# Kernel optimization log

Hardware: AMD Instinct MI355X
Metric: run time of the kernel (lower is better)

The kernel has to match this reference:

```python
import jax, jax.numpy as jnp
import numpy as np

B, T, E, H, V = 4, 2048, 1024, 16, 32000
HD = E // H  # head_dim = 64


def setup_inputs() -> dict:
    key = jax.random.key(0)
    ks = jax.random.split(key, 16)
    s = 0.02
    p = lambda k, shp: jax.random.normal(k, shp, jnp.float32) * s
    return {
        "x": jax.random.randint(ks[0], (B, T), 0, V),
        "tok_emb": p(ks[1], (V, E)),
        "pos_emb": p(ks[2], (T, E)),
        "m_Wq": p(ks[3], (E, E)), "m_Wk": p(ks[4], (E, E)),
        "m_Wv": p(ks[5], (E, E)), "m_Wo": p(ks[6], (E, E)),
        "m_bo": jnp.zeros((E,), jnp.float32),
        "h_Wq": p(ks[7], (E, E)), "h_Wk": p(ks[8], (E, E)),
        "h_Wv": p(ks[9], (E, E)), "h_Wo": p(ks[10], (E, E)),
        "h_bo": jnp.zeros((E,), jnp.float32),
        "f_W1": p(ks[11], (E, 512)), "f_b1": jnp.zeros((512,), jnp.float32),
        "f_W2": p(ks[12], (512, 1024)), "f_b2": jnp.zeros((1024,), jnp.float32),
        "f_W3": p(ks[13], (1024, 512)), "f_b3": jnp.zeros((512,), jnp.float32),
        "f_W4": p(ks[14], (512, E)), "f_b4": jnp.zeros((E,), jnp.float32),
        "ln_g": jnp.ones((E,), jnp.float32),
        "ln_b": jnp.zeros((E,), jnp.float32),
    }


def _layernorm(x, g, b, eps=1e-5):
    m = x.mean(-1, keepdims=True)
    v = ((x - m) ** 2).mean(-1, keepdims=True)
    return (x - m) / jnp.sqrt(v + eps) * g + b


def _mha(x, Wq, Wk, Wv, Wo, bo, masked):
    b, t, e = x.shape
    # [b, t, e] -> [b, h, t, hd]
    q = (x @ Wq).reshape(b, t, H, HD).transpose(0, 2, 1, 3)
    k = (x @ Wk).reshape(b, t, H, HD).transpose(0, 2, 1, 3)
    v = (x @ Wv).reshape(b, t, H, HD).transpose(0, 2, 1, 3)
    wei = jnp.einsum("bhqd,bhkd->bhqk", q, k) / np.float32(np.sqrt(HD))
    if masked:  # causal (module is in training mode by default)
        causal = jnp.tril(jnp.ones((t, t), dtype=bool))
        wei = jnp.where(causal, wei, -jnp.inf)
    att = jax.nn.softmax(wei, axis=-1)
    out = jnp.einsum("bhqk,bhkd->bhqd", att, v).transpose(0, 2, 1, 3).reshape(b, t, e)
    return out @ Wo + bo


def _ffn(x, W1, b1, W2, b2, W3, b3, W4, b4):
    h = jax.nn.relu(x @ W1 + b1)
    h = jax.nn.relu(h @ W2 + b2)
    h = jax.nn.relu(h @ W3 + b3)
    return h @ W4 + b4


def reference(x, tok_emb, pos_emb,
              m_Wq, m_Wk, m_Wv, m_Wo, m_bo,
              h_Wq, h_Wk, h_Wv, h_Wo, h_bo,
              f_W1, f_b1, f_W2, f_b2, f_W3, f_b3, f_W4, f_b4,
              ln_g, ln_b):
    e = tok_emb[x] + pos_emb[jnp.arange(x.shape[1])]          # [B, T, E]
    r = _layernorm(e + _mha(e, m_Wq, m_Wk, m_Wv, m_Wo, m_bo, True), ln_g, ln_b)
    r = _layernorm(r + _mha(r, h_Wq, h_Wk, h_Wv, h_Wo, h_bo, False), ln_g, ln_b)
    r = _layernorm(r + _ffn(r, f_W1, f_b1, f_W2, f_b2, f_W3, f_b3, f_W4, f_b4), ln_g, ln_b)
    return r
```

## Files before the change

### kernel.cpp

```cpp
#include <hip/hip_runtime.h>
#include <hip/hip_bf16.h>


typedef __attribute__((ext_vector_type(8))) short v8s;
typedef __attribute__((ext_vector_type(4))) short v4s;
typedef __attribute__((ext_vector_type(4))) float v4f;
typedef __attribute__((ext_vector_type(16))) float v16f;
typedef __attribute__((ext_vector_type(4))) unsigned int v4u;

#define MFMA16(a, b, c) __builtin_amdgcn_mfma_f32_16x16x32_bf16((a), (b), (c), 0, 0, 0)
#define MFMA32(a, b, c) __builtin_amdgcn_mfma_f32_32x32x16_bf16((a), (b), (c), 0, 0, 0)

typedef const __attribute__((address_space(1))) void* gas1_t;
typedef __attribute__((address_space(3))) void* las3_t;

__device__ __forceinline__ void gl_lds16(const void* g, void* l) {
  __builtin_amdgcn_global_load_lds((gas1_t)g, (las3_t)l, 16, 0, 0);
}

__device__ __forceinline__ unsigned short f2bf(float f) {
  __hip_bfloat16 h = __float2bfloat16(f);
  return *reinterpret_cast<unsigned short*>(&h);
}

__device__ __forceinline__ float bf2f(unsigned short u) {
  union { unsigned int i; float f; } v;
  v.i = (unsigned int)u << 16;
  return v.f;
}

__device__ __forceinline__ float fast_exp2(float x) {
  float r;
  asm("v_exp_f32 %0, %1" : "=v"(r) : "v"(x));
  return r;
}

__device__ __forceinline__ unsigned int cvt_pk_bf16(float lo, float hi) {
  unsigned int r;
  asm("v_cvt_pk_bf16_f32 %0, %1, %2" : "=v"(r) : "v"(lo), "v"(hi));
  return r;
}

__device__ __forceinline__ float max3f(float a, float b, float c) {
  float r;
  asm("v_max3_f32 %0, %1, %2, %3" : "=v"(r) : "v"(a), "v"(b), "v"(c));
  return r;
}

#define QSCALE 0.18033688011112042f

struct TransDesc {
  const float* src[12];
  unsigned short* dst[12];
};

__global__ __launch_bounds__(256)
void transpose_all(TransDesc td) {
  const int bid = blockIdx.x;
  int m, tile, K, N;
  if (bid < 8192) { m = bid >> 10; tile = bid & 1023; K = 1024; N = 1024; }
  else {
    const int r = bid - 8192;
    m = 8 + (r >> 9); tile = r & 511;
    if (m & 1) { K = 512; N = 1024; } else { K = 1024; N = 512; }
  }
  const float* src = td.src[m];
  unsigned short* dst = td.dst[m];
  const int ntx = N >> 5;
  const int n0 = (tile % ntx) * 32, k0 = (tile / ntx) * 32;

  __shared__ float tile_s[32][33];
  const int tx = threadIdx.x & 31, ty = threadIdx.x >> 5;
#pragma unroll
  for (int i = 0; i < 32; i += 8)
    tile_s[ty + i][tx] = src[(size_t)(k0 + ty + i) * N + n0 + tx];
  __syncthreads();
#pragma unroll
  for (int i = 0; i < 32; i += 8)
    dst[(size_t)(n0 + ty + i) * K + k0 + tx] = f2bf(tile_s[tx][ty + i]);
}

__global__ __launch_bounds__(256)
void embed_k(const int* __restrict__ x, const float* __restrict__ tok,
             const float* __restrict__ pos, unsigned short* __restrict__ act) {
  const int t = blockIdx.x, tid = threadIdx.x;
  const int id = x[t], tp = t & 2047;
  float4 v = ((const float4*)(tok + (size_t)id * 1024))[tid];
  float4 p = ((const float4*)(pos + (size_t)tp * 1024))[tid];
  ushort4 u;
  u.x = f2bf(v.x + p.x); u.y = f2bf(v.y + p.y);
  u.z = f2bf(v.z + p.z); u.w = f2bf(v.w + p.w);
  ((ushort4*)(act + (size_t)t * 1024))[tid] = u;
}

__global__ __launch_bounds__(256)
void gemm_bt(const unsigned short* __restrict__ A, const unsigned short* __restrict__ Bt,
             const float* __restrict__ bias, void* __restrict__ C,
             int M, int N, int K, int flags) {
  __shared__ __align__(16) unsigned short As[128 * 64];
  __shared__ __align__(16) unsigned short Bs[128 * 64];
  const int tid = threadIdx.x;
  const int w = tid >> 6, l = tid & 63;
  const int l31 = l & 31, l5 = l >> 5;
  const int wm = w & 1, wn = w >> 1;
  const int m0 = blockIdx.x * 128, n0 = blockIdx.y * 128;
  const int ra = l >> 3, ka = ((l & 7) ^ (l >> 3)) * 8;
  const int fswz = (l31 & 7) * 8;

  v16f acc[2][2];
#pragma unroll
  for (int bm = 0; bm < 2; ++bm)
#pragma unroll
    for (int bn = 0; bn < 2; ++bn)
#pragma unroll
      for (int r = 0; r < 16; ++r) acc[bm][bn][r] = 0.f;

  for (int k0 = 0; k0 < K; k0 += 64) {
#pragma unroll
    for (int i = 0; i < 4; ++i) {
      const int c = w + i * 4;
      gl_lds16(A  + (size_t)(m0 + c * 8 + ra) * K + k0 + ka, &As[c * 512]);
      gl_lds16(Bt + (size_t)(n0 + c * 8 + ra) * K + k0 + ka, &Bs[c * 512]);
    }
    __syncthreads();
#pragma unroll
    for (int kk = 0; kk < 4; ++kk) {
      const int co = (kk * 16 + l5 * 8) ^ fswz;
      const v8s a0 = *(const v8s*)&As[(wm * 64 + l31) * 64 + co];
      const v8s a1 = *(const v8s*)&As[(wm * 64 + 32 + l31) * 64 + co];
      const v8s b0 = *(const v8s*)&Bs[(wn * 64 + l31) * 64 + co];
      const v8s b1 = *(const v8s*)&Bs[(wn * 64 + 32 + l31) * 64 + co];
      acc[0][0] = MFMA32(a0, b0, acc[0][0]);
      acc[0][1] = MFMA32(a0, b1, acc[0][1]);
      acc[1][0] = MFMA32(a1, b0, acc[1][0]);
      acc[1][1] = MFMA32(a1, b1, acc[1][1]);
    }
    __syncthreads();
  }

  const bool relu = flags & 1, obf = flags & 2, qs = flags & 4;
#pragma unroll
  for (int bn = 0; bn < 2; ++bn) {
    const int col = n0 + wn * 64 + bn * 32 + l31;
    const float bv = bias ? bias[col] : 0.f;
    const float sc = (qs && col < 1024) ? QSCALE : 1.f;
#pragma unroll
    for (int bm = 0; bm < 2; ++bm) {
      const int rowbase = m0 + wm * 64 + bm * 32 + 4 * l5;
#pragma unroll
      for (int r = 0; r < 16; ++r) {
        const int row = rowbase + (r & 3) + 8 * (r >> 2);
        float v = (acc[bm][bn][r] + bv) * sc;
        if (relu) v = fmaxf(v, 0.f);
        if (obf) ((unsigned short*)C)[(size_t)row * N + col] = f2bf(v);
        else     ((float*)C)[(size_t)row * N + col] = v;
      }
    }
  }
}

#define LDQ 3072
template <bool CAUSAL>
__global__ __launch_bounds__(512)
void flash_attn(const unsigned short* __restrict__ qkv, unsigned short* __restrict__ O) {
  __shared__ __align__(16) unsigned short Kt[64 * 64];
  __shared__ __align__(16) unsigned short Vt[64 * 64];
  const int tid = threadIdx.x;
  const int w = tid >> 6, l = tid & 63, lr = l & 15, lg = l >> 4;
  const int b = blockIdx.y >> 4, h = blockIdx.y & 15;
  const size_t baseq = ((size_t)b * 2048) * LDQ + h * 64;
  const size_t baseo = ((size_t)b * 2048) * 1024 + h * 64;
  const int kswz = (lr & 7) * 8;
  const int vswz = lr * 4;

  const int kra = l >> 3, kka = ((l & 7) ^ (l >> 3)) * 8;
  const int vp_ = tid & 31, vd0 = ((tid >> 5) & 7) * 8;

  const int nq = CAUSAL ? 2 : 1;
  for (int qi = 0; qi < nq; ++qi) {
    const int qt = CAUSAL ? (qi ? 15 - (int)blockIdx.x : (int)blockIdx.x)
                          : (int)blockIdx.x;
    const int q0w = qt * 128 + w * 16;

    const unsigned short* qp = qkv + baseq + (size_t)(q0w + lr) * LDQ + lg * 8;
    const v8s qf0 = *(const v8s*)qp;
    const v8s qf1 = *(const v8s*)(qp + 32);

    v4f acc[4];
    const v4f vzero = {0.f, 0.f, 0.f, 0.f};
#pragma unroll
    for (int n = 0; n < 4; ++n) acc[n] = vzero;
    float mrow = -INFINITY, lrow = 0.f;

    const int kv_end = CAUSAL ? qt * 128 + 128 : 2048;
    for (int kv0 = 0; kv0 < kv_end; kv0 += 64) {
      if (w >= 4) {
#pragma unroll
        for (int i = 0; i < 2; ++i) {
          const int c = (w - 4) * 2 + i;
          gl_lds16(qkv + baseq + 1024 + (size_t)(kv0 + c * 8 + kra) * LDQ + kka,
                   &Kt[c * 512]);
        }
      } else {
        const unsigned short* va = qkv + baseq + 2048 + (size_t)(kv0 + 2 * vp_) * LDQ + vd0;
        const v8s v0 = *(const v8s*)va;
        const v8s v1 = *(const v8s*)(va + LDQ);
#pragma unroll
        for (int j = 0; j < 8; ++j) {
          const unsigned int pk = (unsigned int)(unsigned short)v0[j] |
                                  ((unsigned int)(unsigned short)v1[j] << 16);
          *(unsigned int*)&Vt[(vd0 + j) * 64 + ((2 * vp_) ^ (((vd0 + j) & 15) * 4))] = pk;
        }
      }
      __syncthreads();

      v4f s[4];
#pragma unroll
      for (int n = 0; n < 4; ++n) s[n] = vzero;
      __builtin_amdgcn_s_setprio(1);
#pragma unroll
      for (int kk = 0; kk < 2; ++kk) {
#pragma unroll
        for (int n = 0; n < 4; ++n) {
          const v8s kf = *(const v8s*)&Kt[(n * 16 + lr) * 64 + ((kk * 32 + lg * 8) ^ kswz)];
          s[n] = MFMA16(kf, kk ? qf1 : qf0, s[n]);
        }
      }
      __builtin_amdgcn_s_setprio(0);

      if (CAUSAL && (kv0 + 63 > q0w)) {
        const int qg = q0w + lr;
#pragma unroll
        for (int n = 0; n < 4; ++n) {
          const int kvb = kv0 + n * 16 + lg * 4;
#pragma unroll
          for (int r = 0; r < 4; ++r)
            if (kvb + r > qg) s[n][r] = -INFINITY;
        }
      }

      float tm;
      {
        const float t0 = max3f(s[0][0], s[0][1], s[0][2]);
        const float t1 = max3f(s[0][3], s[1][0], s[1][1]);
        const float t2 = max3f(s[1][2], s[1][3], s[2][0]);
        const float t3 = max3f(s[2][1], s[2][2], s[2][3]);
        const float t4 = max3f(s[3][0], s[3][1], s[3][2]);
        tm = max3f(t0, t1, s[3][3]);
        tm = max3f(tm, t2, t3);
        tm = fmaxf(tm, t4);
      }
      tm = fmaxf(tm, __shfl_xor(tm, 16));
      tm = fmaxf(tm, __shfl_xor(tm, 32));

      if (__any(tm > mrow + 8.f)) {
        const float mn = fmaxf(mrow, tm);
        const float fac = fast_exp2(mrow - mn);
        mrow = mn;
        lrow *= fac;
        float facT[4];
#pragma unroll
        for (int r = 0; r < 4; ++r)
          facT[r] = __shfl(fac, (l & 48) | (lg * 4 + r));
#pragma unroll
        for (int n = 0; n < 4; ++n)
#pragma unroll
          for (int r = 0; r < 4; ++r) acc[n][r] *= facT[r];
      }

      float rs = 0.f;
#pragma unroll
      for (int n = 0; n < 4; ++n)
#pragma unroll
        for (int r = 0; r < 4; ++r) {
          s[n][r] = fast_exp2(s[n][r] - mrow);
          rs += s[n][r];
        }
      rs += __shfl_xor(rs, 16);
      rs += __shfl_xor(rs, 32);
      lrow += rs;

      v4u pu0, pu1;
      pu0.x = cvt_pk_bf16(s[0][0], s[0][1]); pu0.y = cvt_pk_bf16(s[0][2], s[0][3]);
      pu0.z = cvt_pk_bf16(s[1][0], s[1][1]); pu0.w = cvt_pk_bf16(s[1][2], s[1][3]);
      pu1.x = cvt_pk_bf16(s[2][0], s[2][1]); pu1.y = cvt_pk_bf16(s[2][2], s[2][3]);
      pu1.z = cvt_pk_bf16(s[3][0], s[3][1]); pu1.w = cvt_pk_bf16(s[3][2], s[3][3]);
      v8s pf0, pf1;
      __builtin_memcpy(&pf0, &pu0, 16);
      __builtin_memcpy(&pf1, &pu1, 16);

      __builtin_amdgcn_s_setprio(1);
#pragma unroll
      for (int kk = 0; kk < 2; ++kk) {
#pragma unroll
        for (int n = 0; n < 4; ++n) {
          const int rowb = (n * 16 + lr) * 64;
          const v4s va_ = *(const v4s*)&Vt[rowb + ((kk * 32 + lg * 4) ^ vswz)];
          const v4s vb_ = *(const v4s*)&Vt[rowb + ((kk * 32 + 16 + lg * 4) ^ vswz)];
          const v8s vf = __builtin_shufflevector(va_, vb_, 0, 1, 2, 3, 4, 5, 6, 7);
          acc[n] = MFMA16(kk ? pf1 : pf0, vf, acc[n]);
        }
      }
      __builtin_amdgcn_s_setprio(0);
      __syncthreads();
    }

    float lT[4];
#pragma unroll
    for (int r = 0; r < 4; ++r)
      lT[r] = __shfl(lrow, (l & 48) | (lg * 4 + r));
#pragma unroll
    for (int n = 0; n < 4; ++n)
#pragma unroll
      for (int r = 0; r < 4; ++r) {
        const float v = acc[n][r] / lT[r];
        O[baseo + (size_t)(q0w + lg * 4 + r) * 1024 + n * 16 + lr] = f2bf(v);
      }
  }
}

__global__ __launch_bounds__(256)
void add_ln(const unsigned short* __restrict__ ra, const unsigned short* __restrict__ rb,
            const float* __restrict__ g, const float* __restrict__ be,
            unsigned short* __restrict__ ob, float* __restrict__ of) {
  const int t = blockIdx.x, tid = threadIdx.x;
  const ushort4 ua = ((const ushort4*)(ra + (size_t)t * 1024))[tid];
  const ushort4 ub = ((const ushort4*)(rb + (size_t)t * 1024))[tid];
  float4 s;
  s.x = bf2f(ua.x) + bf2f(ub.x);
  s.y = bf2f(ua.y) + bf2f(ub.y);
  s.z = bf2f(ua.z) + bf2f(ub.z);
  s.w = bf2f(ua.w) + bf2f(ub.w);
  float sum = s.x + s.y + s.z + s.w;
  float sq  = s.x * s.x + s.y * s.y + s.z * s.z + s.w * s.w;
#pragma unroll
  for (int off = 32; off > 0; off >>= 1) {
    sum += __shfl_xor(sum, off);
    sq  += __shfl_xor(sq, off);
  }
  __shared__ float red[8];
  const int w = tid >> 6;
  if ((tid & 63) == 0) { red[w] = sum; red[4 + w] = sq; }
  __syncthreads();
  sum = red[0] + red[1] + red[2] + red[3];
  sq  = red[4] + red[5] + red[6] + red[7];
  const float mean = sum * (1.f / 1024.f);
  const float var  = sq * (1.f / 1024.f) - mean * mean;
  const float rstd = rsqrtf(var + 1e-5f);
  const float4 gg = ((const float4*)g)[tid];
  const float4 bb = ((const float4*)be)[tid];
  float4 y;
  y.x = (s.x - mean) * rstd * gg.x + bb.x;
  y.y = (s.y - mean) * rstd * gg.y + bb.y;
  y.z = (s.z - mean) * rstd * gg.z + bb.z;
  y.w = (s.w - mean) * rstd * gg.w + bb.w;
  if (ob) {
    ushort4 u;
    u.x = f2bf(y.x); u.y = f2bf(y.y); u.z = f2bf(y.z); u.w = f2bf(y.w);
    ((ushort4*)(ob + (size_t)t * 1024))[tid] = u;
  }
  if (of) ((float4*)(of + (size_t)t * 1024))[tid] = y;
}

extern "C" void kernel_launch(void* const* d_in, const int* in_sizes, int n_in,
                              void* d_out, int out_size, void* d_ws, size_t ws_size,
                              hipStream_t stream) {
  const int*   x    = (const int*)d_in[0];
  const float* tok  = (const float*)d_in[1];
  const float* pos  = (const float*)d_in[2];
  const float* mWq  = (const float*)d_in[3];
  const float* mWk  = (const float*)d_in[4];
  const float* mWv  = (const float*)d_in[5];
  const float* mWo  = (const float*)d_in[6];
  const float* m_bo = (const float*)d_in[7];
  const float* hWq  = (const float*)d_in[8];
  const float* hWk  = (const float*)d_in[9];
  const float* hWv  = (const float*)d_in[10];
  const float* hWo  = (const float*)d_in[11];
  const float* h_bo = (const float*)d_in[12];
  const float* fW1  = (const float*)d_in[13];
  const float* f_b1 = (const float*)d_in[14];
  const float* fW2  = (const float*)d_in[15];
  const float* f_b2 = (const float*)d_in[16];
  const float* fW3  = (const float*)d_in[17];
  const float* f_b3 = (const float*)d_in[18];
  const float* fW4  = (const float*)d_in[19];
  const float* f_b4 = (const float*)d_in[20];
  const float* ln_g = (const float*)d_in[21];
  const float* ln_b = (const float*)d_in[22];

  char* ws = (char*)d_ws;
  const size_t MB = 1ull << 20;
  unsigned short* wqkv1 = (unsigned short*)(ws + 0 * MB);
  unsigned short* wqkv2 = (unsigned short*)(ws + 6 * MB);
  unsigned short* wo1   = (unsigned short*)(ws + 12 * MB);
  unsigned short* wo2   = (unsigned short*)(ws + 14 * MB);
  unsigned short* fW1_t = (unsigned short*)(ws + 16 * MB);
  unsigned short* fW2_t = (unsigned short*)(ws + 17 * MB);
  unsigned short* fW3_t = (unsigned short*)(ws + 18 * MB);
  unsigned short* fW4_t = (unsigned short*)(ws + 19 * MB);
  unsigned short* actA  = (unsigned short*)(ws + 20 * MB);
  unsigned short* actB  = (unsigned short*)(ws + 36 * MB);
  unsigned short* tmp   = (unsigned short*)(ws + 52 * MB);
  unsigned short* qkv   = (unsigned short*)(ws + 68 * MB);
  unsigned short* h1    = (unsigned short*)(ws + 68 * MB);
  unsigned short* h2    = (unsigned short*)(ws + 76 * MB);
  unsigned short* h3    = (unsigned short*)(ws + 92 * MB);
  unsigned short* attno = (unsigned short*)(ws + 116 * MB);

  TransDesc td;
  td.src[0] = mWq; td.dst[0] = wqkv1;
  td.src[1] = mWk; td.dst[1] = wqkv1 + 1024 * 1024;
  td.src[2] = mWv; td.dst[2] = wqkv1 + 2048 * 1024;
  td.src[3] = mWo; td.dst[3] = wo1;
  td.src[4] = hWq; td.dst[4] = wqkv2;
  td.src[5] = hWk; td.dst[5] = wqkv2 + 1024 * 1024;
  td.src[6] = hWv; td.dst[6] = wqkv2 + 2048 * 1024;
  td.src[7] = hWo; td.dst[7] = wo2;
  td.src[8] = fW1; td.dst[8] = fW1_t;
  td.src[9] = fW2; td.dst[9] = fW2_t;
  td.src[10] = fW3; td.dst[10] = fW3_t;
  td.src[11] = fW4; td.dst[11] = fW4_t;
  transpose_all<<<10240, 256, 0, stream>>>(td);

  embed_k<<<8192, 256, 0, stream>>>(x, tok, pos, actA);

  gemm_bt<<<dim3(64, 24), 256, 0, stream>>>(actA, wqkv1, nullptr, qkv, 8192, 3072, 1024, 6);
  flash_attn<true><<<dim3(8, 64), 512, 0, stream>>>(qkv, attno);
  gemm_bt<<<dim3(64, 8), 256, 0, stream>>>(attno, wo1, m_bo, tmp, 8192, 1024, 1024, 2);
  add_ln<<<8192, 256, 0, stream>>>(actA, tmp, ln_g, ln_b, actB, nullptr);

  gemm_bt<<<dim3(64, 24), 256, 0, stream>>>(actB, wqkv2, nullptr, qkv, 8192, 3072, 1024, 6);
  flash_attn<false><<<dim3(16, 64), 512, 0, stream>>>(qkv, attno);
  gemm_bt<<<dim3(64, 8), 256, 0, stream>>>(attno, wo2, h_bo, tmp, 8192, 1024, 1024, 2);
  add_ln<<<8192, 256, 0, stream>>>(actB, tmp, ln_g, ln_b, actA, nullptr);

  gemm_bt<<<dim3(64, 4), 256, 0, stream>>>(actA, fW1_t, f_b1, h1, 8192, 512, 1024, 3);
  gemm_bt<<<dim3(64, 8), 256, 0, stream>>>(h1, fW2_t, f_b2, h2, 8192, 1024, 512, 3);
  gemm_bt<<<dim3(64, 4), 256, 0, stream>>>(h2, fW3_t, f_b3, h3, 8192, 512, 1024, 3);
  gemm_bt<<<dim3(64, 8), 256, 0, stream>>>(h3, fW4_t, f_b4, tmp, 8192, 1024, 512, 2);
  add_ln<<<8192, 256, 0, stream>>>(actA, tmp, ln_g, ln_b, nullptr, (float*)d_out);
}
```

Before: 504.1 us.

## Double-buffer K/V tiles in flash attention to overlap loads with compute

Splits the K and V shared-memory tiles into two buffers and prefetches the next kv tile while the current one is used for QK^T, softmax and PV. K goes straight to LDS through global_load_lds, and V is loaded into registers early and written transposed after the softmax. This drops one barrier per iteration and hides global load latency, at the cost of twice the LDS and more live registers.

```diff
diff --git a/kernel.cpp b/kernel.cpp
--- a/kernel.cpp
+++ b/kernel.cpp
@@ -163,8 +163,8 @@
 template <bool CAUSAL>
 __global__ __launch_bounds__(512)
 void flash_attn(const unsigned short* __restrict__ qkv, unsigned short* __restrict__ O) {
-  __shared__ __align__(16) unsigned short Kt[64 * 64];
-  __shared__ __align__(16) unsigned short Vt[64 * 64];
+  __shared__ __align__(16) unsigned short Kt[2][64 * 64];
+  __shared__ __align__(16) unsigned short Vt[2][64 * 64];
   const int tid = threadIdx.x;
   const int w = tid >> 6, l = tid & 63, lr = l & 15, lg = l >> 4;
   const int b = blockIdx.y >> 4, h = blockIdx.y & 15;
@@ -175,6 +175,8 @@
 
   const int kra = l >> 3, kka = ((l & 7) ^ (l >> 3)) * 8;
   const int vp_ = tid & 31, vd0 = ((tid >> 5) & 7) * 8;
+  const unsigned short* Kbase = qkv + baseq + 1024 + (size_t)kra * LDQ + kka;
+  const unsigned short* Vbase = qkv + baseq + 2048 + (size_t)(2 * vp_) * LDQ + vd0;
 
   const int nq = CAUSAL ? 2 : 1;
   for (int qi = 0; qi < nq; ++qi) {
@@ -193,26 +195,43 @@
     float mrow = -INFINITY, lrow = 0.f;
 
     const int kv_end = CAUSAL ? qt * 128 + 128 : 2048;
+
+    if (w >= 4) {
+#pragma unroll
+      for (int i = 0; i < 2; ++i) {
+        const int c = (w - 4) * 2 + i;
+        gl_lds16(Kbase + (size_t)(c * 8) * LDQ, &Kt[0][c * 512]);
+      }
+    } else {
+      const v8s v0 = *(const v8s*)Vbase;
+      const v8s v1 = *(const v8s*)(Vbase + LDQ);
+#pragma unroll
+      for (int j = 0; j < 8; ++j) {
+        const unsigned int pk = (unsigned int)(unsigned short)v0[j] |
+                                ((unsigned int)(unsigned short)v1[j] << 16);
+        *(unsigned int*)&Vt[0][(vd0 + j) * 64 + ((2 * vp_) ^ (((vd0 + j) & 15) * 4))] = pk;
+      }
+    }
+    __syncthreads();
+
+    int cur = 0;
     for (int kv0 = 0; kv0 < kv_end; kv0 += 64) {
+      const bool have = (kv0 + 64) < kv_end;
+      v8s nv0, nv1;
       if (w >= 4) {
-#pragma unroll
-        for (int i = 0; i < 2; ++i) {
-          const int c = (w - 4) * 2 + i;
-          gl_lds16(qkv + baseq + 1024 + (size_t)(kv0 + c * 8 + kra) * LDQ + kka,
-                   &Kt[c * 512]);
-        }
-      } else {
-        const unsigned short* va = qkv + baseq + 2048 + (size_t)(kv0 + 2 * vp_) * LDQ + vd0;
-        const v8s v0 = *(const v8s*)va;
-        const v8s v1 = *(const v8s*)(va + LDQ);
-#pragma unroll
-        for (int j = 0; j < 8; ++j) {
-          const unsigned int pk = (unsigned int)(unsigned short)v0[j] |
-                                  ((unsigned int)(unsigned short)v1[j] << 16);
-          *(unsigned int*)&Vt[(vd0 + j) * 64 + ((2 * vp_) ^ (((vd0 + j) & 15) * 4))] = pk;
-        }
-      }
-      __syncthreads();
+        if (have) {
+          const int nxt = kv0 + 64;
+#pragma unroll
+          for (int i = 0; i < 2; ++i) {
+            const int c = (w - 4) * 2 + i;
+            gl_lds16(Kbase + (size_t)(nxt + c * 8) * LDQ, &Kt[cur ^ 1][c * 512]);
+          }
+        }
+      } else if (have) {
+        const unsigned short* va = Vbase + (size_t)(kv0 + 64) * LDQ;
+        nv0 = *(const v8s*)va;
+        nv1 = *(const v8s*)(va + LDQ);
+      }
 
       v4f s[4];
 #pragma unroll
@@ -222,7 +241,7 @@
       for (int kk = 0; kk < 2; ++kk) {
 #pragma unroll
         for (int n = 0; n < 4; ++n) {
-          const v8s kf = *(const v8s*)&Kt[(n * 16 + lr) * 64 + ((kk * 32 + lg * 8) ^ kswz)];
+          const v8s kf = *(const v8s*)&Kt[cur][(n * 16 + lr) * 64 + ((kk * 32 + lg * 8) ^ kswz)];
           s[n] = MFMA16(kf, kk ? qf1 : qf0, s[n]);
         }
       }
@@ -280,6 +299,15 @@
       rs += __shfl_xor(rs, 32);
       lrow += rs;
 
+      if (w < 4 && have) {
+#pragma unroll
+        for (int j = 0; j < 8; ++j) {
+          const unsigned int pk = (unsigned int)(unsigned short)nv0[j] |
+                                  ((unsigned int)(unsigned short)nv1[j] << 16);
+          *(unsigned int*)&Vt[cur ^ 1][(vd0 + j) * 64 + ((2 * vp_) ^ (((vd0 + j) & 15) * 4))] = pk;
+        }
+      }
+
       v4u pu0, pu1;
       pu0.x = cvt_pk_bf16(s[0][0], s[0][1]); pu0.y = cvt_pk_bf16(s[0][2], s[0][3]);
       pu0.z = cvt_pk_bf16(s[1][0], s[1][1]); pu0.w = cvt_pk_bf16(s[1][2], s[1][3]);
@@ -295,14 +323,15 @@
 #pragma unroll
         for (int n = 0; n < 4; ++n) {
           const int rowb = (n * 16 + lr) * 64;
-          const v4s va_ = *(const v4s*)&Vt[rowb + ((kk * 32 + lg * 4) ^ vswz)];
-          const v4s vb_ = *(const v4s*)&Vt[rowb + ((kk * 32 + 16 + lg * 4) ^ vswz)];
+          const v4s va_ = *(const v4s*)&Vt[cur][rowb + ((kk * 32 + lg * 4) ^ vswz)];
+          const v4s vb_ = *(const v4s*)&Vt[cur][rowb + ((kk * 32 + 16 + lg * 4) ^ vswz)];
           const v8s vf = __builtin_shufflevector(va_, vb_, 0, 1, 2, 3, 4, 5, 6, 7);
           acc[n] = MFMA16(kk ? pf1 : pf0, vf, acc[n]);
         }
       }
       __builtin_amdgcn_s_setprio(0);
       __syncthreads();
+      cur ^= 1;
     }
 
     float lT[4];
```

Result: faster. 489.0 us (-3.0%).
